# Kernel optimization log

Measured on AMD Instinct MI355X. Metric: run time of the kernel, lower is better.

The kernel has to match this reference:

```python
import jax, jax.numpy as jnp
import numpy as np

N, F, C1, H, C2, E = 50000, 256, 32, 8, 16, 800000
NEG_SLOPE = 0.2


def gat_layer(x, src, dst, W, a_src, a_dst, b, heads, out_c, concat):
    n = x.shape[0]
    h = (x @ W).reshape(n, heads, out_c)               # [N,H,C]
    al_src = jnp.sum(h * a_src, axis=-1)               # [N,H]
    al_dst = jnp.sum(h * a_dst, axis=-1)               # [N,H]
    e = jax.nn.leaky_relu(al_src[src] + al_dst[dst], NEG_SLOPE)  # [E,H]
    # segment softmax over incoming edges of each dst node
    m = jax.ops.segment_max(e, dst, num_segments=n)
    e = jnp.exp(e - m[dst])
    denom = jax.ops.segment_sum(e, dst, num_segments=n)
    alpha = e / (denom[dst] + 1e-16)                   # [E,H]
    msg = h[src] * alpha[..., None]                    # [E,H,C]
    out = jax.ops.segment_sum(msg, dst, num_segments=n)
    out = out.reshape(n, heads * out_c) if concat else out.mean(axis=1)
    return out + b


def conv1d(x, w, b):
    # x: [1,C,N], w: [O,I,K], 'same' padding (K=5 -> pad 2)
    pad = (w.shape[-1] - 1) // 2
    y = jax.lax.conv_general_dilated(x, w, (1,), [(pad, pad)],
                                     dimension_numbers=('NCH', 'OIH', 'NCH'))
    return y + b[None, :, None]


def setup_inputs() -> dict:
    key = jax.random.key(0)
    ks = jax.random.split(key, 20)
    s = lambda k, shp, sc: jax.random.normal(k, shp, jnp.float32) * sc
    inp = {
        'x': jax.random.normal(ks[0], (N, F), jnp.float32),
        'edge_index': jax.random.randint(ks[1], (2, E), 0, N, jnp.int32),
        'W1': s(ks[2], (F, H * C1), 0.06),
        'a_src1': s(ks[3], (H, C1), 0.1), 'a_dst1': s(ks[4], (H, C1), 0.1),
        'b1': jnp.zeros((H * C1,), jnp.float32),
        'W2': s(ks[5], (H * C1, C2), 0.06),
        'a_src2': s(ks[6], (1, C2), 0.1), 'a_dst2': s(ks[7], (1, C2), 0.1),
        'b2': jnp.zeros((C2,), jnp.float32),
        'proj_w': s(ks[8], (C2, 1), 0.2), 'proj_b': jnp.zeros((1,), jnp.float32),
        'c1_w': s(ks[9], (C2, C2, 5), 0.1), 'c1_b': jnp.zeros((C2,), jnp.float32),
        'c2_w': s(ks[10], (C2, C2, 5), 0.1), 'c2_b': jnp.zeros((C2,), jnp.float32),
        'lin_w': s(ks[11], (2 * C2, C2), 0.15), 'lin_b': jnp.zeros((C2,), jnp.float32),
    }
    return inp


def reference(x, edge_index, W1, a_src1, a_dst1, b1, W2, a_src2, a_dst2, b2,
              proj_w, proj_b, c1_w, c1_b, c2_w, c2_b, lin_w, lin_b):
    n = x.shape[0]
    loops = jnp.arange(n, dtype=edge_index.dtype)
    src = jnp.concatenate([edge_index[0], loops])  # PyG GATConv adds self-loops
    dst = jnp.concatenate([edge_index[1], loops])

    h = jax.nn.relu(gat_layer(x, src, dst, W1, a_src1, a_dst1, b1, H, C1, True))
    x1 = gat_layer(h, src, dst, W2, a_src2, a_dst2, b2, 1, C2, False)  # [N,C2]

    g = (x1 @ proj_w + proj_b)[:, 0]                  # [N]
    sort_idx = jnp.argsort(g)
    inverse_idx = jnp.argsort(sort_idx)
    sorted_x = g[sort_idx][:, None] * x1[sort_idx]    # [N,C2]
    sx = sorted_x.T[None]                             # [1,C2,N]
    sx = jax.nn.relu(conv1d(sx, c1_w, c1_b))
    sx = conv1d(sx, c2_w, c2_b)
    x2 = sx[0].T[inverse_idx]                         # [N,C2]

    out = jnp.concatenate([x1, x2], axis=1) @ lin_w + lin_b
    return jax.nn.log_softmax(out, axis=1)
```

## Files before the change

### kernel.cpp

```cpp
#include <hip/hip_runtime.h>
#include <math.h>

#define NBUCKET 65536

__device__ __forceinline__ float leakyrelu02(float v) { return v > 0.f ? v : 0.2f * v; }

__global__ __launch_bounds__(256) void k_gemm1(const float* __restrict__ A,
                                               const float* __restrict__ B,
                                               float* __restrict__ C,
                                               const float* __restrict__ a_src,
                                               const float* __restrict__ a_dst,
                                               float* __restrict__ als,
                                               float* __restrict__ ald, int M) {
  __shared__ float As[16][68];
  __shared__ float pS[64][4];
  __shared__ float pD[64][4];
  const int m0 = blockIdx.x * 64;
  const int n0 = blockIdx.y * 64;
  const int tid = threadIdx.x;
  const int l = tid & 63;
  const int wu = __builtin_amdgcn_readfirstlane(tid >> 6);
  const float* __restrict__ Bw = B + n0 + wu * 16;

  float acc[16];
#pragma unroll
  for (int j = 0; j < 16; ++j) acc[j] = 0.f;

  const int arow = tid & 63, akk = (tid >> 6) * 4;

  for (int k0 = 0; k0 < 256; k0 += 16) {
    float4 av = make_float4(0.f, 0.f, 0.f, 0.f);
    if (m0 + arow < M) av = *(const float4*)(A + (size_t)(m0 + arow) * 256 + k0 + akk);
    As[akk + 0][arow] = av.x;
    As[akk + 1][arow] = av.y;
    As[akk + 2][arow] = av.z;
    As[akk + 3][arow] = av.w;
    __syncthreads();
#pragma unroll
    for (int kk = 0; kk < 16; ++kk) {
      const float* bp = Bw + (size_t)(k0 + kk) * 256;
      float4 b0 = *(const float4*)(bp);
      float4 b1 = *(const float4*)(bp + 4);
      float4 b2 = *(const float4*)(bp + 8);
      float4 b3 = *(const float4*)(bp + 12);
      float a = As[kk][l];
      acc[0] += a * b0.x;  acc[1] += a * b0.y;  acc[2] += a * b0.z;  acc[3] += a * b0.w;
      acc[4] += a * b1.x;  acc[5] += a * b1.y;  acc[6] += a * b1.z;  acc[7] += a * b1.w;
      acc[8] += a * b2.x;  acc[9] += a * b2.y;  acc[10] += a * b2.z; acc[11] += a * b2.w;
      acc[12] += a * b3.x; acc[13] += a * b3.y; acc[14] += a * b3.z; acc[15] += a * b3.w;
    }
    __syncthreads();
  }
  const int m = m0 + l;
  if (m < M) {
    float* cp = C + (size_t)m * 256 + n0 + wu * 16;
    *(float4*)(cp + 0) = make_float4(acc[0], acc[1], acc[2], acc[3]);
    *(float4*)(cp + 4) = make_float4(acc[4], acc[5], acc[6], acc[7]);
    *(float4*)(cp + 8) = make_float4(acc[8], acc[9], acc[10], acc[11]);
    *(float4*)(cp + 12) = make_float4(acc[12], acc[13], acc[14], acc[15]);
  }

  const int hseg = n0 >> 5;
  const int aoff = (hseg + (wu >> 1)) * 32 + (wu & 1) * 16;
  float ps = 0.f, pd = 0.f;
#pragma unroll
  for (int j = 0; j < 16; ++j) {
    ps += acc[j] * a_src[aoff + j];
    pd += acc[j] * a_dst[aoff + j];
  }
  pS[l][wu] = ps;
  pD[l][wu] = pd;
  __syncthreads();
  if (tid < 128) {
    int row = tid & 63, hp = tid >> 6;
    int mm = m0 + row;
    if (mm < M) {
      als[(size_t)mm * 8 + hseg + hp] = pS[row][hp * 2] + pS[row][hp * 2 + 1];
      ald[(size_t)mm * 8 + hseg + hp] = pD[row][hp * 2] + pD[row][hp * 2 + 1];
    }
  }
}

__global__ __launch_bounds__(256) void k_hist(const int* __restrict__ ei,
                                              int* __restrict__ counts, int E, int N) {
  int e = blockIdx.x * 256 + threadIdx.x;
  if (e >= E + N) return;
  int d = (e < E) ? ei[E + e] : (e - E);
  atomicAdd(&counts[d], 1);
}

__global__ __launch_bounds__(1024) void k_scan(const int* __restrict__ counts,
                                               int* __restrict__ offsets,
                                               int* __restrict__ cursor, int chunk) {
  __shared__ int part[1024];
  const int t = threadIdx.x;
  const int base = t * chunk;
  int ssum = 0;
  for (int i = 0; i < chunk; i += 4) {
    int4 v = *(const int4*)(counts + base + i);
    ssum += v.x + v.y + v.z + v.w;
  }
  part[t] = ssum;
  __syncthreads();
  for (int d = 1; d < 1024; d <<= 1) {
    int v = (t >= d) ? part[t - d] : 0;
    __syncthreads();
    part[t] += v;
    __syncthreads();
  }
  int run = (t == 0) ? 0 : part[t - 1];
  for (int i = 0; i < chunk; i += 4) {
    int4 v = *(const int4*)(counts + base + i);
    int4 o;
    o.x = run; run += v.x;
    o.y = run; run += v.y;
    o.z = run; run += v.z;
    o.w = run; run += v.w;
    *(int4*)(offsets + base + i) = o;
    if (cursor) *(int4*)(cursor + base + i) = o;
  }
  if (t == 1023) offsets[1024 * chunk] = run;
}

__global__ __launch_bounds__(256) void k_scatter_ew(
    const int* __restrict__ ei, const float* __restrict__ als1,
    const float* __restrict__ ald1, int* __restrict__ cursor,
    int* __restrict__ csr_src, float* __restrict__ ew, int E, int N) {
  int e = blockIdx.x * 256 + threadIdx.x;
  if (e >= E + N) return;
  int d, s;
  if (e < E) { d = ei[E + e]; s = ei[e]; }
  else { d = e - E; s = d; }
  int pos = atomicAdd(&cursor[d], 1);
  csr_src[pos] = s;
  float4 as0 = *(const float4*)(als1 + (size_t)s * 8);
  float4 as1 = *(const float4*)(als1 + (size_t)s * 8 + 4);
  float4 ad0 = *(const float4*)(ald1 + (size_t)d * 8);
  float4 ad1 = *(const float4*)(ald1 + (size_t)d * 8 + 4);
  float4 w0, w1;
  w0.x = expf(leakyrelu02(as0.x + ad0.x));
  w0.y = expf(leakyrelu02(as0.y + ad0.y));
  w0.z = expf(leakyrelu02(as0.z + ad0.z));
  w0.w = expf(leakyrelu02(as0.w + ad0.w));
  w1.x = expf(leakyrelu02(as1.x + ad1.x));
  w1.y = expf(leakyrelu02(as1.y + ad1.y));
  w1.z = expf(leakyrelu02(as1.z + ad1.z));
  w1.w = expf(leakyrelu02(as1.w + ad1.w));
  *(float4*)(ew + (size_t)pos * 8) = w0;
  *(float4*)(ew + (size_t)pos * 8 + 4) = w1;
}

#define RB(i) ((i) + ((i) >> 3))

__global__ __launch_bounds__(256) void k_gat1(
    const float* __restrict__ h_lin, const float* __restrict__ ew,
    const float* __restrict__ b1, const int* __restrict__ offsets,
    const int* __restrict__ csr_src, const float* __restrict__ W2,
    const float* __restrict__ a_src2, const float* __restrict__ a_dst2,
    float* __restrict__ h2, float* __restrict__ als2, float* __restrict__ ald2, int N) {
  __shared__ float rowbuf[4][292];

  const int w = threadIdx.x >> 6;
  const int l = threadIdx.x & 63;
  const int half = l >> 5;
  const int li = l & 31;
  const int h3 = li >> 2;
  const int n = blockIdx.x * 4 + w;
  if (n >= N) return;

  const int off = offsets[n];
  const int deg = offsets[n + 1] - off;
  const float* hb = h_lin + li * 8;

  float c0 = 0.f, c1 = 0.f, c2 = 0.f, c3 = 0.f, c4 = 0.f, c5 = 0.f, c6 = 0.f, c7 = 0.f;
  float sw = 0.f;
  int e = 0;
  for (; e + 8 <= deg; e += 8) {
    const int p0 = off + e + half;
    int s0 = csr_src[p0];
    int s1 = csr_src[p0 + 2];
    int s2 = csr_src[p0 + 4];
    int s3 = csr_src[p0 + 6];
    float w0 = ew[(size_t)p0 * 8 + h3];
    float w1 = ew[(size_t)(p0 + 2) * 8 + h3];
    float w2v = ew[(size_t)(p0 + 4) * 8 + h3];
    float w3 = ew[(size_t)(p0 + 6) * 8 + h3];
    const float* r0p = hb + (size_t)s0 * 256;
    const float* r1p = hb + (size_t)s1 * 256;
    const float* r2p = hb + (size_t)s2 * 256;
    const float* r3p = hb + (size_t)s3 * 256;
    float4 r0a = *(const float4*)(r0p), r0b = *(const float4*)(r0p + 4);
    float4 r1a = *(const float4*)(r1p), r1b = *(const float4*)(r1p + 4);
    float4 r2a = *(const float4*)(r2p), r2b = *(const float4*)(r2p + 4);
    float4 r3a = *(const float4*)(r3p), r3b = *(const float4*)(r3p + 4);
    sw += (w0 + w1) + (w2v + w3);
    c0 += w0 * r0a.x + w1 * r1a.x + w2v * r2a.x + w3 * r3a.x;
    c1 += w0 * r0a.y + w1 * r1a.y + w2v * r2a.y + w3 * r3a.y;
    c2 += w0 * r0a.z + w1 * r1a.z + w2v * r2a.z + w3 * r3a.z;
    c3 += w0 * r0a.w + w1 * r1a.w + w2v * r2a.w + w3 * r3a.w;
    c4 += w0 * r0b.x + w1 * r1b.x + w2v * r2b.x + w3 * r3b.x;
    c5 += w0 * r0b.y + w1 * r1b.y + w2v * r2b.y + w3 * r3b.y;
    c6 += w0 * r0b.z + w1 * r1b.z + w2v * r2b.z + w3 * r3b.z;
    c7 += w0 * r0b.w + w1 * r1b.w + w2v * r2b.w + w3 * r3b.w;
  }
  for (; e < deg; e += 2) {
    int ee = e + half;
    if (ee < deg) {
      int p = off + ee;
      int s = csr_src[p];
      float ww = ew[(size_t)p * 8 + h3];
      const float* rp = hb + (size_t)s * 256;
      float4 ra = *(const float4*)(rp), rb = *(const float4*)(rp + 4);
      sw += ww;
      c0 += ww * ra.x; c1 += ww * ra.y; c2 += ww * ra.z; c3 += ww * ra.w;
      c4 += ww * rb.x; c5 += ww * rb.y; c6 += ww * rb.z; c7 += ww * rb.w;
    }
  }
  c0 += __shfl_xor(c0, 32); c1 += __shfl_xor(c1, 32);
  c2 += __shfl_xor(c2, 32); c3 += __shfl_xor(c3, 32);
  c4 += __shfl_xor(c4, 32); c5 += __shfl_xor(c5, 32);
  c6 += __shfl_xor(c6, 32); c7 += __shfl_xor(c7, 32);
  sw += __shfl_xor(sw, 32);
  const float inv = 1.f / (sw + 1e-16f);

  if (half == 0) {
    float4 ba = *(const float4*)(b1 + li * 8);
    float4 bbv = *(const float4*)(b1 + li * 8 + 4);
    rowbuf[w][RB(li * 8 + 0)] = fmaxf(c0 * inv + ba.x, 0.f);
    rowbuf[w][RB(li * 8 + 1)] = fmaxf(c1 * inv + ba.y, 0.f);
    rowbuf[w][RB(li * 8 + 2)] = fmaxf(c2 * inv + ba.z, 0.f);
    rowbuf[w][RB(li * 8 + 3)] = fmaxf(c3 * inv + ba.w, 0.f);
    rowbuf[w][RB(li * 8 + 4)] = fmaxf(c4 * inv + bbv.x, 0.f);
    rowbuf[w][RB(li * 8 + 5)] = fmaxf(c5 * inv + bbv.y, 0.f);
    rowbuf[w][RB(li * 8 + 6)] = fmaxf(c6 * inv + bbv.z, 0.f);
    rowbuf[w][RB(li * 8 + 7)] = fmaxf(c7 * inv + bbv.w, 0.f);
  }
  asm volatile("s_waitcnt lgkmcnt(0)" ::: "memory");

  const int o = l & 15;
  const int grp = l >> 4;
  float a2 = 0.f;
#pragma unroll 8
  for (int t = 0; t < 64; ++t) {
    int cc = grp * 64 + ((t + grp * 8) & 63);
    a2 += rowbuf[w][RB(cc)] * W2[cc * 16 + o];
  }
  a2 += __shfl_xor(a2, 16);
  a2 += __shfl_xor(a2, 32);

  if (l < 16) {
    h2[(size_t)n * 16 + l] = a2;
    float ps = a2 * a_src2[l];
    float pd = a2 * a_dst2[l];
    ps += __shfl_xor(ps, 1); pd += __shfl_xor(pd, 1);
    ps += __shfl_xor(ps, 2); pd += __shfl_xor(pd, 2);
    ps += __shfl_xor(ps, 4); pd += __shfl_xor(pd, 4);
    ps += __shfl_xor(ps, 8); pd += __shfl_xor(pd, 8);
    if (l == 0) { als2[n] = ps; ald2[n] = pd; }
  }
}

__global__ __launch_bounds__(256) void k_gat2(
    const float* __restrict__ h2, const float* __restrict__ als2,
    const float* __restrict__ ald2, const float* __restrict__ b2,
    const float* __restrict__ proj_w, const float* __restrict__ proj_b,
    const int* __restrict__ offsets, const int* __restrict__ csr_src,
    float* __restrict__ x1, float* __restrict__ g,
    unsigned long long* __restrict__ keys, int* __restrict__ bhist, int N) {
  const int w = threadIdx.x >> 6;
  const int l = threadIdx.x & 63;
  const int n = blockIdx.x * 4 + w;
  if (n >= N) return;
  const int off = offsets[n];
  const int deg = offsets[n + 1] - off;
  const float ad = ald2[n];
  const int slot = l >> 4;
  const int c = l & 15;

  float acc = 0.f, sw = 0.f;
  int e0 = 0;
  for (; e0 + 8 <= deg; e0 += 8) {
    int pA = off + e0 + slot;
    int pB = off + e0 + 4 + slot;
    int sA = csr_src[pA];
    int sB = csr_src[pB];
    float vA = als2[sA];
    float vB = als2[sB];
    float hA = h2[(size_t)sA * 16 + c];
    float hB = h2[(size_t)sB * 16 + c];
    float wA = expf(leakyrelu02(vA + ad));
    float wB = expf(leakyrelu02(vB + ad));
    sw += wA + wB;
    acc += wA * hA + wB * hB;
  }
  for (; e0 < deg; e0 += 4) {
    int e = e0 + slot;
    if (e < deg) {
      int p = off + e;
      int s = csr_src[p];
      float v = expf(leakyrelu02(als2[s] + ad));
      sw += v;
      acc += v * h2[(size_t)s * 16 + c];
    }
  }
  acc += __shfl_xor(acc, 16); sw += __shfl_xor(sw, 16);
  acc += __shfl_xor(acc, 32); sw += __shfl_xor(sw, 32);
  float x1v = acc / (sw + 1e-16f) + b2[c];

  float pg = x1v * proj_w[c];
  pg += __shfl_xor(pg, 1);
  pg += __shfl_xor(pg, 2);
  pg += __shfl_xor(pg, 4);
  pg += __shfl_xor(pg, 8);
  if (l < 16) x1[(size_t)n * 16 + l] = x1v;
  if (l == 0) {
    float gv = pg + proj_b[0];
    g[n] = gv;
    unsigned u = __float_as_uint(gv);
    u = (u & 0x80000000u) ? ~u : (u | 0x80000000u);
    keys[n] = (((unsigned long long)u) << 32) | (unsigned)n;
    atomicAdd(&bhist[u >> 16], 1);
  }
}

__global__ __launch_bounds__(256) void k_bscatter(const unsigned long long* __restrict__ keys,
                                                  int* __restrict__ cursor,
                                                  unsigned long long* __restrict__ bkeys, int N) {
  int n = blockIdx.x * 256 + threadIdx.x;
  if (n >= N) return;
  unsigned long long k = keys[n];
  int b = (int)(k >> 48);
  int pos = atomicAdd(&cursor[b], 1);
  bkeys[pos] = k;
}

__global__ __launch_bounds__(256) void k_brank(const unsigned long long* __restrict__ bkeys,
                                               const int* __restrict__ boffs,
                                               const float* __restrict__ g,
                                               const float* __restrict__ x1,
                                               int* __restrict__ rank,
                                               float* __restrict__ sortedv, int N) {
  int pos = blockIdx.x * 256 + threadIdx.x;
  if (pos >= N) return;
  unsigned long long k = bkeys[pos];
  int b = (int)(k >> 48);
  int lo = boffs[b], hi = boffs[b + 1];
  int r = lo;
  for (int j = lo; j < hi; ++j) r += (bkeys[j] < k) ? 1 : 0;
  int idx = (int)(unsigned)(k & 0xffffffffull);
  rank[idx] = r;
  float gv = g[idx];
#pragma unroll
  for (int c = 0; c < 16; c += 4) {
    float4 v = *(const float4*)(x1 + (size_t)idx * 16 + c);
    float4 o = make_float4(gv * v.x, gv * v.y, gv * v.z, gv * v.w);
    *(float4*)(sortedv + (size_t)r * 16 + c) = o;
  }
}

__global__ __launch_bounds__(256) void k_conv(const float* __restrict__ in,
                                              const float* __restrict__ wgt,
                                              const float* __restrict__ bias,
                                              float* __restrict__ out, int N, int relu) {
  __shared__ float s[260][17];
  __shared__ float ws[1280];
  __shared__ float bs[16];
  const int p0 = blockIdx.x * 256;
  for (int i = threadIdx.x; i < 1280; i += 256) ws[i] = wgt[i];
  if (threadIdx.x < 16) bs[threadIdx.x] = bias[threadIdx.x];
  for (int idx = threadIdx.x; idx < 260 * 16; idx += 256) {
    int lp = idx >> 4, c = idx & 15;
    int gp = p0 - 2 + lp;
    s[lp][c] = (gp >= 0 && gp < N) ? in[(size_t)gp * 16 + c] : 0.f;
  }
  __syncthreads();
  const int p = p0 + threadIdx.x;
  if (p >= N) return;
  float acc[16];
#pragma unroll
  for (int o = 0; o < 16; ++o) acc[o] = bs[o];
  for (int k = 0; k < 5; ++k) {
    for (int c = 0; c < 16; ++c) {
      float xv = s[threadIdx.x + k][c];
#pragma unroll
      for (int o = 0; o < 16; ++o) acc[o] += ws[(o * 16 + c) * 5 + k] * xv;
    }
  }
#pragma unroll
  for (int o = 0; o < 16; ++o) {
    float v = acc[o];
    if (relu) v = fmaxf(v, 0.f);
    out[(size_t)p * 16 + o] = v;
  }
}

__global__ __launch_bounds__(256) void k_final(
    const float* __restrict__ x1, const float* __restrict__ c2out,
    const int* __restrict__ rank, const float* __restrict__ lin_w,
    const float* __restrict__ lin_b, float* __restrict__ out, int N) {
  __shared__ float lw[512];
  __shared__ float lb[16];
  for (int i = threadIdx.x; i < 512; i += 256) lw[i] = lin_w[i];
  if (threadIdx.x < 16) lb[threadIdx.x] = lin_b[threadIdx.x];
  __syncthreads();
  const int n = blockIdx.x * 256 + threadIdx.x;
  if (n >= N) return;
  float xa[16], xb[16];
  const int r = rank[n];
#pragma unroll
  for (int c = 0; c < 16; c += 4) {
    float4 va = *(const float4*)(x1 + (size_t)n * 16 + c);
    float4 vb = *(const float4*)(c2out + (size_t)r * 16 + c);
    xa[c] = va.x; xa[c + 1] = va.y; xa[c + 2] = va.z; xa[c + 3] = va.w;
    xb[c] = vb.x; xb[c + 1] = vb.y; xb[c + 2] = vb.z; xb[c + 3] = vb.w;
  }
  float z[16];
#pragma unroll
  for (int o = 0; o < 16; ++o) z[o] = lb[o];
#pragma unroll
  for (int c = 0; c < 16; ++c) {
    float va = xa[c], vb = xb[c];
#pragma unroll
    for (int o = 0; o < 16; ++o) z[o] += va * lw[c * 16 + o] + vb * lw[(16 + c) * 16 + o];
  }
  float m = z[0];
#pragma unroll
  for (int o = 1; o < 16; ++o) m = fmaxf(m, z[o]);
  float ssum = 0.f;
#pragma unroll
  for (int o = 0; o < 16; ++o) ssum += expf(z[o] - m);
  float lse = m + logf(ssum);
#pragma unroll
  for (int o = 0; o < 16; ++o) out[(size_t)n * 16 + o] = z[o] - lse;
}

extern "C" void kernel_launch(void* const* d_in, const int* in_sizes, int n_in,
                              void* d_out, int out_size, void* d_ws, size_t ws_size,
                              hipStream_t stream) {
  const float* x = (const float*)d_in[0];
  const int* ei = (const int*)d_in[1];
  const float* W1 = (const float*)d_in[2];
  const float* a_src1 = (const float*)d_in[3];
  const float* a_dst1 = (const float*)d_in[4];
  const float* b1 = (const float*)d_in[5];
  const float* W2 = (const float*)d_in[6];
  const float* a_src2 = (const float*)d_in[7];
  const float* a_dst2 = (const float*)d_in[8];
  const float* b2 = (const float*)d_in[9];
  const float* proj_w = (const float*)d_in[10];
  const float* proj_b = (const float*)d_in[11];
  const float* c1_w = (const float*)d_in[12];
  const float* c1_b = (const float*)d_in[13];
  const float* c2_w = (const float*)d_in[14];
  const float* c2_b = (const float*)d_in[15];
  const float* lin_w = (const float*)d_in[16];
  const float* lin_b = (const float*)d_in[17];
  float* out = (float*)d_out;

  const int N = in_sizes[0] / 256;
  const int E = in_sizes[1] / 2;
  const int Etot = E + N;

  int chunk = (N + 1023) / 1024;
  chunk = (chunk + 3) & ~3;
  const int Npad = 1024 * chunk;

  char* ws = (char*)d_ws;
  size_t off = 0;
  auto alloc = [&](size_t bytes) -> void* {
    void* p = ws + off;
    off = (off + bytes + 255) & ~(size_t)255;
    return p;
  };
  float* h_lin = (float*)alloc((size_t)N * 256 * 4);
  float* als1 = (float*)alloc((size_t)N * 8 * 4);
  float* ald1 = (float*)alloc((size_t)N * 8 * 4);
  int* counts = (int*)alloc((size_t)Npad * 4);
  int* offsets = (int*)alloc((size_t)(Npad + 1) * 4);
  int* cursor = (int*)alloc((size_t)Npad * 4);
  int* csr_src = (int*)alloc((size_t)Etot * 4);
  float* ew = (float*)alloc((size_t)Etot * 8 * 4);
  float* h2 = (float*)alloc((size_t)N * 16 * 4);
  float* als2 = (float*)alloc((size_t)N * 4);
  float* ald2 = (float*)alloc((size_t)N * 4);
  float* x1 = (float*)alloc((size_t)N * 16 * 4);
  float* gbuf = (float*)alloc((size_t)N * 4);
  unsigned long long* keys = (unsigned long long*)alloc((size_t)N * 8);
  int* bhist = (int*)alloc((size_t)NBUCKET * 4);
  int* boffs = (int*)alloc((size_t)(NBUCKET + 1) * 4);
  int* bcursor = (int*)alloc((size_t)NBUCKET * 4);
  unsigned long long* bkeys = (unsigned long long*)alloc((size_t)N * 8);
  int* rank = (int*)alloc((size_t)N * 4);
  float* sortedv = (float*)alloc((size_t)N * 16 * 4);
  float* c1out = (float*)alloc((size_t)N * 16 * 4);
  float* c2out = (float*)alloc((size_t)N * 16 * 4);
  if (off > ws_size) return;

  hipMemsetAsync(counts, 0, (size_t)Npad * 4, stream);
  hipMemsetAsync(bhist, 0, (size_t)NBUCKET * 4, stream);

  dim3 gg((N + 63) / 64, 4);
  k_gemm1<<<gg, 256, 0, stream>>>(x, W1, h_lin, a_src1, a_dst1, als1, ald1, N);
  k_hist<<<(Etot + 255) / 256, 256, 0, stream>>>(ei, counts, E, N);
  k_scan<<<1, 1024, 0, stream>>>(counts, offsets, cursor, chunk);
  k_scatter_ew<<<(Etot + 255) / 256, 256, 0, stream>>>(ei, als1, ald1, cursor,
                                                       csr_src, ew, E, N);
  k_gat1<<<(N + 3) / 4, 256, 0, stream>>>(h_lin, ew, b1, offsets, csr_src,
                                          W2, a_src2, a_dst2, h2, als2, ald2, N);
  k_gat2<<<(N + 3) / 4, 256, 0, stream>>>(h2, als2, ald2, b2, proj_w, proj_b,
                                          offsets, csr_src, x1, gbuf, keys, bhist, N);
  k_scan<<<1, 1024, 0, stream>>>(bhist, boffs, bcursor, NBUCKET / 1024);
  k_bscatter<<<(N + 255) / 256, 256, 0, stream>>>(keys, bcursor, bkeys, N);
  k_brank<<<(N + 255) / 256, 256, 0, stream>>>(bkeys, boffs, gbuf, x1, rank, sortedv, N);
  k_conv<<<(N + 255) / 256, 256, 0, stream>>>(sortedv, c1_w, c1_b, c1out, N, 1);
  k_conv<<<(N + 255) / 256, 256, 0, stream>>>(c1out, c2_w, c2_b, c2out, N, 0);
  k_final<<<(N + 255) / 256, 256, 0, stream>>>(x1, c2out, rank, lin_w, lin_b, out, N);
}
```

Baseline: 533.9 us.

## Fuse two conv1d kernels, shrink sort buckets, batch B loads in gemm1

Merges the two conv1d launches into one kernel that computes the relu'd first conv into shared memory (with halo recompute of 4 extra rows) and then the second conv, removing an intermediate global buffer and a launch. Reduces the bucket-sort histogram from 65536 to 16384 buckets, which makes the scan cheaper but puts more keys in each bucket, so the per-bucket linear rank loop does more work. Restructures the gemm1 inner loop to load four rows of B before the FMAs to expose more memory-level parallelism, at the cost of more registers.

```diff
diff --git a/kernel.cpp b/kernel.cpp
--- a/kernel.cpp
+++ b/kernel.cpp
@@ -1,7 +1,7 @@
 #include <hip/hip_runtime.h>
 #include <math.h>
 
-#define NBUCKET 65536
+#define NBUCKET 16384
 
 __device__ __forceinline__ float leakyrelu02(float v) { return v > 0.f ? v : 0.2f * v; }
 
@@ -37,17 +37,31 @@
     As[akk + 3][arow] = av.w;
     __syncthreads();
 #pragma unroll
-    for (int kk = 0; kk < 16; ++kk) {
-      const float* bp = Bw + (size_t)(k0 + kk) * 256;
-      float4 b0 = *(const float4*)(bp);
-      float4 b1 = *(const float4*)(bp + 4);
-      float4 b2 = *(const float4*)(bp + 8);
-      float4 b3 = *(const float4*)(bp + 12);
-      float a = As[kk][l];
-      acc[0] += a * b0.x;  acc[1] += a * b0.y;  acc[2] += a * b0.z;  acc[3] += a * b0.w;
-      acc[4] += a * b1.x;  acc[5] += a * b1.y;  acc[6] += a * b1.z;  acc[7] += a * b1.w;
-      acc[8] += a * b2.x;  acc[9] += a * b2.y;  acc[10] += a * b2.z; acc[11] += a * b2.w;
-      acc[12] += a * b3.x; acc[13] += a * b3.y; acc[14] += a * b3.z; acc[15] += a * b3.w;
+    for (int g = 0; g < 4; ++g) {
+      float4 b[4][4];
+#pragma unroll
+      for (int q = 0; q < 4; ++q) {
+        const float* bp = Bw + (size_t)(k0 + g * 4 + q) * 256;
+        b[q][0] = *(const float4*)(bp);
+        b[q][1] = *(const float4*)(bp + 4);
+        b[q][2] = *(const float4*)(bp + 8);
+        b[q][3] = *(const float4*)(bp + 12);
+      }
+      float a_[4];
+#pragma unroll
+      for (int q = 0; q < 4; ++q) a_[q] = As[g * 4 + q][l];
+#pragma unroll
+      for (int q = 0; q < 4; ++q) {
+        float a = a_[q];
+        acc[0] += a * b[q][0].x;  acc[1] += a * b[q][0].y;
+        acc[2] += a * b[q][0].z;  acc[3] += a * b[q][0].w;
+        acc[4] += a * b[q][1].x;  acc[5] += a * b[q][1].y;
+        acc[6] += a * b[q][1].z;  acc[7] += a * b[q][1].w;
+        acc[8] += a * b[q][2].x;  acc[9] += a * b[q][2].y;
+        acc[10] += a * b[q][2].z; acc[11] += a * b[q][2].w;
+        acc[12] += a * b[q][3].x; acc[13] += a * b[q][3].y;
+        acc[14] += a * b[q][3].z; acc[15] += a * b[q][3].w;
+      }
     }
     __syncthreads();
   }
@@ -319,7 +333,7 @@
     unsigned u = __float_as_uint(gv);
     u = (u & 0x80000000u) ? ~u : (u | 0x80000000u);
     keys[n] = (((unsigned long long)u) << 32) | (unsigned)n;
-    atomicAdd(&bhist[u >> 16], 1);
+    atomicAdd(&bhist[u >> 18], 1);
   }
 }
 
@@ -329,7 +343,7 @@
   int n = blockIdx.x * 256 + threadIdx.x;
   if (n >= N) return;
   unsigned long long k = keys[n];
-  int b = (int)(k >> 48);
+  int b = (int)(k >> 50);
   int pos = atomicAdd(&cursor[b], 1);
   bkeys[pos] = k;
 }
@@ -343,7 +357,7 @@
   int pos = blockIdx.x * 256 + threadIdx.x;
   if (pos >= N) return;
   unsigned long long k = bkeys[pos];
-  int b = (int)(k >> 48);
+  int b = (int)(k >> 50);
   int lo = boffs[b], hi = boffs[b + 1];
   int r = lo;
   for (int j = lo; j < hi; ++j) r += (bkeys[j] < k) ? 1 : 0;
@@ -358,40 +372,59 @@
   }
 }
 
-__global__ __launch_bounds__(256) void k_conv(const float* __restrict__ in,
-                                              const float* __restrict__ wgt,
-                                              const float* __restrict__ bias,
-                                              float* __restrict__ out, int N, int relu) {
-  __shared__ float s[260][17];
-  __shared__ float ws[1280];
-  __shared__ float bs[16];
+__global__ __launch_bounds__(256) void k_conv12(const float* __restrict__ in,
+                                                const float* __restrict__ w1,
+                                                const float* __restrict__ bias1,
+                                                const float* __restrict__ w2,
+                                                const float* __restrict__ bias2,
+                                                float* __restrict__ out, int N) {
+  __shared__ float s[264][17];
+  __shared__ float c1s[260][17];
+  __shared__ float w1s[1280];
+  __shared__ float w2s[1280];
+  __shared__ float b1s[16];
+  __shared__ float b2s[16];
   const int p0 = blockIdx.x * 256;
-  for (int i = threadIdx.x; i < 1280; i += 256) ws[i] = wgt[i];
-  if (threadIdx.x < 16) bs[threadIdx.x] = bias[threadIdx.x];
-  for (int idx = threadIdx.x; idx < 260 * 16; idx += 256) {
+  const int t = threadIdx.x;
+  for (int i = t; i < 1280; i += 256) { w1s[i] = w1[i]; w2s[i] = w2[i]; }
+  if (t < 16) { b1s[t] = bias1[t]; b2s[t] = bias2[t]; }
+  for (int idx = t; idx < 264 * 16; idx += 256) {
     int lp = idx >> 4, c = idx & 15;
-    int gp = p0 - 2 + lp;
+    int gp = p0 - 4 + lp;
     s[lp][c] = (gp >= 0 && gp < N) ? in[(size_t)gp * 16 + c] : 0.f;
   }
   __syncthreads();
-  const int p = p0 + threadIdx.x;
+  for (int r = t; r < 260; r += 256) {
+    int q = p0 - 2 + r;
+    float a1[16];
+#pragma unroll
+    for (int o = 0; o < 16; ++o) a1[o] = b1s[o];
+    for (int k = 0; k < 5; ++k) {
+      for (int c = 0; c < 16; ++c) {
+        float xv = s[r + k][c];
+#pragma unroll
+        for (int o = 0; o < 16; ++o) a1[o] += w1s[(o * 16 + c) * 5 + k] * xv;
+      }
+    }
+    bool inb = (q >= 0 && q < N);
+#pragma unroll
+    for (int o = 0; o < 16; ++o) c1s[r][o] = inb ? fmaxf(a1[o], 0.f) : 0.f;
+  }
+  __syncthreads();
+  const int p = p0 + t;
   if (p >= N) return;
-  float acc[16];
-#pragma unroll
-  for (int o = 0; o < 16; ++o) acc[o] = bs[o];
+  float a2[16];
+#pragma unroll
+  for (int o = 0; o < 16; ++o) a2[o] = b2s[o];
   for (int k = 0; k < 5; ++k) {
     for (int c = 0; c < 16; ++c) {
-      float xv = s[threadIdx.x + k][c];
-#pragma unroll
-      for (int o = 0; o < 16; ++o) acc[o] += ws[(o * 16 + c) * 5 + k] * xv;
+      float xv = c1s[t + k][c];
+#pragma unroll
+      for (int o = 0; o < 16; ++o) a2[o] += w2s[(o * 16 + c) * 5 + k] * xv;
     }
   }
 #pragma unroll
-  for (int o = 0; o < 16; ++o) {
-    float v = acc[o];
-    if (relu) v = fmaxf(v, 0.f);
-    out[(size_t)p * 16 + o] = v;
-  }
+  for (int o = 0; o < 16; ++o) out[(size_t)p * 16 + o] = a2[o];
 }
 
 __global__ __launch_bounds__(256) void k_final(
@@ -492,7 +525,6 @@
   unsigned long long* bkeys = (unsigned long long*)alloc((size_t)N * 8);
   int* rank = (int*)alloc((size_t)N * 4);
   float* sortedv = (float*)alloc((size_t)N * 16 * 4);
-  float* c1out = (float*)alloc((size_t)N * 16 * 4);
   float* c2out = (float*)alloc((size_t)N * 16 * 4);
   if (off > ws_size) return;
 
@@ -512,7 +544,6 @@
   k_scan<<<1, 1024, 0, stream>>>(bhist, boffs, bcursor, NBUCKET / 1024);
   k_bscatter<<<(N + 255) / 256, 256, 0, stream>>>(keys, bcursor, bkeys, N);
   k_brank<<<(N + 255) / 256, 256, 0, stream>>>(bkeys, boffs, gbuf, x1, rank, sortedv, N);
-  k_conv<<<(N + 255) / 256, 256, 0, stream>>>(sortedv, c1_w, c1_b, c1out, N, 1);
-  k_conv<<<(N + 255) / 256, 256, 0, stream>>>(c1out, c2_w, c2_b, c2out, N, 0);
+  k_conv12<<<(N + 255) / 256, 256, 0, stream>>>(sortedv, c1_w, c1_b, c2_w, c2_b, c2out, N);
   k_final<<<(N + 255) / 256, 256, 0, stream>>>(x1, c2out, rank, lin_w, lin_b, out, N);
 }
```

Result: slower. 665.8 us (+24.7%).
